# Optimization experiments

Hardware: AMD Instinct MI355X
Metric: run time of the kernel (lower is better)

## Reference

```python
import jax, jax.numpy as jnp
import numpy as np

GAMMA = 0.99  # init kwarg


def _discounted_returns(ep_rs):
    # reversed running_add = running_add*gamma + r, emitted per step
    def step(carry, r):
        carry = carry * GAMMA + r
        return carry, carry
    _, out = jax.lax.scan(step, jnp.float32(0.0), ep_rs, reverse=True)
    return out  # [T]


def setup_inputs() -> dict:
    key = jax.random.key(0)
    k1, k2, k3 = jax.random.split(key, 3)
    T, A = 2097152, 18
    weight = jax.random.normal(k1, (T, A), dtype=jnp.float32)
    ep_rs = jax.random.normal(k2, (T,), dtype=jnp.float32)
    ep_as = jax.random.randint(k3, (T,), 0, A, dtype=jnp.int64)
    return {"weight": weight, "ep_rs": ep_rs, "ep_as": ep_as}


def reference(weight, ep_rs, ep_as):
    d = _discounted_returns(ep_rs)
    d = d - jnp.mean(d)
    # cross_entropy with reduction='none': -log_softmax(weight)[t, ep_as[t]]
    logp = jax.nn.log_softmax(weight, axis=-1)  # [T, A]
    neg_log_prob = -jnp.take_along_axis(logp, ep_as[:, None], axis=-1)[:, 0]  # [T]
    return jnp.mean(neg_log_prob * d)
```

## Files before the change

kernel.cpp:

```cpp
#include <hip/hip_runtime.h>
#include <math.h>

#define T_TOTAL 2097152
#define A_DIM   18
#define GAMMA_D 0.99

#define CHUNK 256
#define NC    (T_TOTAL / CHUNK)
#define KTR   14

#define NB_MAIN 2048

__global__ void k_local(const float* __restrict__ r, double* __restrict__ L) {
    const int tid  = blockIdx.x * blockDim.x + threadIdx.x;
    const int c    = tid >> 6;
    const int lane = tid & 63;
    const float4 v = ((const float4*)r)[(size_t)c * 64 + lane];
    const double g = GAMMA_D;
    double w = pow(g, (double)(4 * lane)) *
               ((double)v.x + g * ((double)v.y + g * ((double)v.z + g * (double)v.w)));
    #pragma unroll
    for (int off = 32; off > 0; off >>= 1) w += __shfl_down(w, off, 64);
    if (lane == 0) L[c] = w;
}

__global__ void k_carry(const double* __restrict__ L, double* __restrict__ carry,
                        double G) {
    const int c = blockIdx.x * blockDim.x + threadIdx.x;
    double acc = 0.0, w = 1.0;
    #pragma unroll
    for (int m = 0; m < KTR; ++m) {
        int idx = c + 1 + m;
        if (idx < NC) acc += w * L[idx];
        w *= G;
    }
    carry[c] = acc;
}

__launch_bounds__(256)
__global__ void k_main(const float* __restrict__ wgt, const int* __restrict__ act,
                       const float* __restrict__ r, const double* __restrict__ carry,
                       double* __restrict__ partials) {
    __shared__ float  lds[CHUNK * A_DIM];
    __shared__ double ldsT[4];
    __shared__ double red[12];
    const int tid  = threadIdx.x;
    const int lane = tid & 63, wv = tid >> 6;
    const double g    = GAMMA_D;
    const double p    = pow(g, (double)tid);
    const double ip   = 1.0 / p;
    const double g256 = pow(g, 256.0);
    double s_d = 0.0, s_n = 0.0, s_nd = 0.0;

    for (int c = blockIdx.x; c < NC; c += gridDim.x) {
        __syncthreads();
        const float4* src = (const float4*)(wgt + (size_t)c * CHUNK * A_DIM);
        float4* dst = (float4*)lds;
        #pragma unroll
        for (int i = 0; i < 5; ++i) {
            int idx = tid + 256 * i;
            if (idx < CHUNK * A_DIM / 4) dst[idx] = src[idx];
        }
        const int row = c * CHUNK + tid;
        double ss = p * (double)r[row];
        #pragma unroll
        for (int off = 1; off < 64; off <<= 1) {
            double v = __shfl_down(ss, off, 64);
            ss += (lane + off < 64) ? v : 0.0;
        }
        if (lane == 0) ldsT[wv] = ss;
        __syncthreads();
        double tail = 0.0;
        #pragma unroll
        for (int m = 0; m < 4; ++m)
            if (m > wv) tail += ldsT[m];
        const double dval = ip * (ss + tail + g256 * carry[c]);
        const float* wr = lds + tid * A_DIM;
        float mx = wr[0];
        #pragma unroll
        for (int j = 1; j < A_DIM; ++j) mx = fmaxf(mx, wr[j]);
        float s = 0.0f;
        #pragma unroll
        for (int j = 0; j < A_DIM; ++j) s += expf(wr[j] - mx);
        const float nlp = mx + logf(s) - wr[act[row]];
        s_d  += dval;
        s_n  += (double)nlp;
        s_nd += (double)nlp * dval;
    }

    #pragma unroll
    for (int off = 32; off > 0; off >>= 1) {
        s_d  += __shfl_down(s_d,  off, 64);
        s_n  += __shfl_down(s_n,  off, 64);
        s_nd += __shfl_down(s_nd, off, 64);
    }
    if (lane == 0) { red[wv*3+0] = s_d; red[wv*3+1] = s_n; red[wv*3+2] = s_nd; }
    __syncthreads();
    if (tid == 0) {
        double a = 0.0, b = 0.0, cc = 0.0;
        #pragma unroll
        for (int i = 0; i < 4; ++i) { a += red[i*3]; b += red[i*3+1]; cc += red[i*3+2]; }
        partials[blockIdx.x*3+0] = a;
        partials[blockIdx.x*3+1] = b;
        partials[blockIdx.x*3+2] = cc;
    }
}

__global__ void k_final(const double* __restrict__ partials, float* __restrict__ out) {
    __shared__ double red[12];
    const int tid = threadIdx.x;
    double a = 0.0, b = 0.0, c = 0.0;
    for (int i = tid; i < NB_MAIN; i += 256) {
        a += partials[i*3+0];
        b += partials[i*3+1];
        c += partials[i*3+2];
    }
    #pragma unroll
    for (int off = 32; off > 0; off >>= 1) {
        a += __shfl_down(a, off, 64);
        b += __shfl_down(b, off, 64);
        c += __shfl_down(c, off, 64);
    }
    const int lane = tid & 63, wv = tid >> 6;
    if (lane == 0) { red[wv*3+0] = a; red[wv*3+1] = b; red[wv*3+2] = c; }
    __syncthreads();
    if (tid == 0) {
        double A_ = 0.0, B_ = 0.0, C_ = 0.0;
        #pragma unroll
        for (int i = 0; i < 4; ++i) { A_ += red[i*3]; B_ += red[i*3+1]; C_ += red[i*3+2]; }
        const double invT = 1.0 / (double)T_TOTAL;
        out[0] = (float)((C_ - (A_ * invT) * B_) * invT);
    }
}

extern "C" void kernel_launch(void* const* d_in, const int* in_sizes, int n_in,
                              void* d_out, int out_size, void* d_ws, size_t ws_size,
                              hipStream_t stream) {
    const float* weight = (const float*)d_in[0];
    const float* ep_rs  = (const float*)d_in[1];
    const int*   ep_as  = (const int*)  d_in[2];
    float* out = (float*)d_out;

    char* ws = (char*)d_ws;
    double* L        = (double*)(ws);
    double* carry    = (double*)(ws + (1 << 16));
    double* partials = (double*)(ws + (2 << 16));

    const double G = pow(GAMMA_D, (double)CHUNK);

    k_local <<<T_TOTAL / 4 / 256, 256, 0, stream>>>(ep_rs, L);
    k_carry <<<NC / 256,          256, 0, stream>>>(L, carry, G);
    k_main  <<<NB_MAIN,           256, 0, stream>>>(weight, ep_as, ep_rs, carry, partials);
    k_final <<<1,                 256, 0, stream>>>(partials, out);
}
```

Before: 234.2 us.

## Fold carry computation into main kernel and fuse final reduction via last-block atomic

Removes the separate carry kernel: each thread in the main kernel recomputes the chunk carry from the per-chunk local sums L, using a 14-term truncated sum. It also removes the final reduction kernel by having the last block to finish, detected through an atomic counter reset in k_local, reduce the partials. The launch count drops from four to two, at the cost of redundant per-thread loads of L in every chunk iteration plus a threadfence and atomic per block.

```diff
diff --git a/kernel.cpp b/kernel.cpp
--- a/kernel.cpp
+++ b/kernel.cpp
@@ -11,8 +11,10 @@
 
 #define NB_MAIN 2048
 
-__global__ void k_local(const float* __restrict__ r, double* __restrict__ L) {
+__global__ void k_local(const float* __restrict__ r, double* __restrict__ L,
+                        unsigned int* __restrict__ done) {
     const int tid  = blockIdx.x * blockDim.x + threadIdx.x;
+    if (tid == 0) *done = 0u;
     const int c    = tid >> 6;
     const int lane = tid & 63;
     const float4 v = ((const float4*)r)[(size_t)c * 64 + lane];
@@ -24,26 +26,16 @@
     if (lane == 0) L[c] = w;
 }
 
-__global__ void k_carry(const double* __restrict__ L, double* __restrict__ carry,
-                        double G) {
-    const int c = blockIdx.x * blockDim.x + threadIdx.x;
-    double acc = 0.0, w = 1.0;
-    #pragma unroll
-    for (int m = 0; m < KTR; ++m) {
-        int idx = c + 1 + m;
-        if (idx < NC) acc += w * L[idx];
-        w *= G;
-    }
-    carry[c] = acc;
-}
-
 __launch_bounds__(256)
 __global__ void k_main(const float* __restrict__ wgt, const int* __restrict__ act,
-                       const float* __restrict__ r, const double* __restrict__ carry,
-                       double* __restrict__ partials) {
+                       const float* __restrict__ r, const double* __restrict__ L,
+                       double* __restrict__ partials,
+                       unsigned int* __restrict__ done,
+                       float* __restrict__ out) {
     __shared__ float  lds[CHUNK * A_DIM];
     __shared__ double ldsT[4];
     __shared__ double red[12];
+    __shared__ unsigned int isLast;
     const int tid  = threadIdx.x;
     const int lane = tid & 63, wv = tid >> 6;
     const double g    = GAMMA_D;
@@ -61,6 +53,13 @@
             int idx = tid + 256 * i;
             if (idx < CHUNK * A_DIM / 4) dst[idx] = src[idx];
         }
+        double cy = 0.0, gw = 1.0;
+        #pragma unroll
+        for (int m = 0; m < KTR; ++m) {
+            int idx = c + 1 + m;
+            if (idx < NC) cy += gw * L[idx];
+            gw *= g256;
+        }
         const int row = c * CHUNK + tid;
         double ss = p * (double)r[row];
         #pragma unroll
@@ -74,7 +73,7 @@
         #pragma unroll
         for (int m = 0; m < 4; ++m)
             if (m > wv) tail += ldsT[m];
-        const double dval = ip * (ss + tail + g256 * carry[c]);
+        const double dval = ip * (ss + tail + g256 * cy);
         const float* wr = lds + tid * A_DIM;
         float mx = wr[0];
         #pragma unroll
@@ -103,33 +102,36 @@
         partials[blockIdx.x*3+0] = a;
         partials[blockIdx.x*3+1] = b;
         partials[blockIdx.x*3+2] = cc;
+        __threadfence();
+        unsigned int prev = atomicAdd(done, 1u);
+        isLast = (prev == (unsigned int)(gridDim.x - 1)) ? 1u : 0u;
     }
-}
+    __syncthreads();
 
-__global__ void k_final(const double* __restrict__ partials, float* __restrict__ out) {
-    __shared__ double red[12];
-    const int tid = threadIdx.x;
-    double a = 0.0, b = 0.0, c = 0.0;
-    for (int i = tid; i < NB_MAIN; i += 256) {
-        a += partials[i*3+0];
-        b += partials[i*3+1];
-        c += partials[i*3+2];
-    }
-    #pragma unroll
-    for (int off = 32; off > 0; off >>= 1) {
-        a += __shfl_down(a, off, 64);
-        b += __shfl_down(b, off, 64);
-        c += __shfl_down(c, off, 64);
-    }
-    const int lane = tid & 63, wv = tid >> 6;
-    if (lane == 0) { red[wv*3+0] = a; red[wv*3+1] = b; red[wv*3+2] = c; }
-    __syncthreads();
-    if (tid == 0) {
-        double A_ = 0.0, B_ = 0.0, C_ = 0.0;
+    if (isLast) {
+        __threadfence();
+        double a = 0.0, b = 0.0, c = 0.0;
+        for (int i = tid; i < NB_MAIN; i += 256) {
+            a += partials[i*3+0];
+            b += partials[i*3+1];
+            c += partials[i*3+2];
+        }
         #pragma unroll
-        for (int i = 0; i < 4; ++i) { A_ += red[i*3]; B_ += red[i*3+1]; C_ += red[i*3+2]; }
-        const double invT = 1.0 / (double)T_TOTAL;
-        out[0] = (float)((C_ - (A_ * invT) * B_) * invT);
+        for (int off = 32; off > 0; off >>= 1) {
+            a += __shfl_down(a, off, 64);
+            b += __shfl_down(b, off, 64);
+            c += __shfl_down(c, off, 64);
+        }
+        __syncthreads();
+        if (lane == 0) { red[wv*3+0] = a; red[wv*3+1] = b; red[wv*3+2] = c; }
+        __syncthreads();
+        if (tid == 0) {
+            double A_ = 0.0, B_ = 0.0, C_ = 0.0;
+            #pragma unroll
+            for (int i = 0; i < 4; ++i) { A_ += red[i*3]; B_ += red[i*3+1]; C_ += red[i*3+2]; }
+            const double invT = 1.0 / (double)T_TOTAL;
+            out[0] = (float)((C_ - (A_ * invT) * B_) * invT);
+        }
     }
 }
 
@@ -142,14 +144,11 @@
     float* out = (float*)d_out;
 
     char* ws = (char*)d_ws;
-    double* L        = (double*)(ws);
-    double* carry    = (double*)(ws + (1 << 16));
-    double* partials = (double*)(ws + (2 << 16));
+    double*       L        = (double*)(ws);
+    double*       partials = (double*)(ws + (1 << 16));
+    unsigned int* done     = (unsigned int*)(ws + (2 << 16));
 
-    const double G = pow(GAMMA_D, (double)CHUNK);
-
-    k_local <<<T_TOTAL / 4 / 256, 256, 0, stream>>>(ep_rs, L);
-    k_carry <<<NC / 256,          256, 0, stream>>>(L, carry, G);
-    k_main  <<<NB_MAIN,           256, 0, stream>>>(weight, ep_as, ep_rs, carry, partials);
-    k_final <<<1,                 256, 0, stream>>>(partials, out);
+    k_local <<<T_TOTAL / 4 / 256, 256, 0, stream>>>(ep_rs, L, done);
+    k_main  <<<NB_MAIN,           256, 0, stream>>>(weight, ep_as, ep_rs, L,
+                                                    partials, done, out);
 }
```

After: 307.9 us. 31.5% more time.

## Launch one block per chunk and replace pow with binary exponentiation

Applied to the files above, without the earlier changes.

The main kernel drops its grid-stride loop and launches one 256-thread block per 256-row chunk, so each block processes exactly one chunk and writes its own partial. The final reduction now sums one partial per chunk. Library pow calls are replaced with an 8-bit square-and-multiply helper and a hard-coded gamma^256 constant, which cuts per-thread setup cost. The change trades the old loop reuse for more blocks in flight, at the cost of a larger partials array and more launch and tail work in the final single-block reduction.

```diff
diff --git a/kernel.cpp b/kernel.cpp
--- a/kernel.cpp
+++ b/kernel.cpp
@@ -9,7 +9,15 @@
 #define NC    (T_TOTAL / CHUNK)
 #define KTR   14
 
-#define NB_MAIN 2048
+__device__ inline void pow_tid(double base, int e, double& out) {
+    double p = 1.0, b = base;
+    #pragma unroll
+    for (int bit = 0; bit < 8; ++bit) {
+        if (e & (1 << bit)) p *= b;
+        b *= b;
+    }
+    out = p;
+}
 
 __global__ void k_local(const float* __restrict__ r, double* __restrict__ L) {
     const int tid  = blockIdx.x * blockDim.x + threadIdx.x;
@@ -17,8 +25,9 @@
     const int lane = tid & 63;
     const float4 v = ((const float4*)r)[(size_t)c * 64 + lane];
     const double g = GAMMA_D;
-    double w = pow(g, (double)(4 * lane)) *
-               ((double)v.x + g * ((double)v.y + g * ((double)v.z + g * (double)v.w)));
+    double p;
+    pow_tid(g, 4 * lane, p);
+    double w = p * ((double)v.x + g * ((double)v.y + g * ((double)v.z + g * (double)v.w)));
     #pragma unroll
     for (int off = 32; off > 0; off >>= 1) w += __shfl_down(w, off, 64);
     if (lane == 0) L[c] = w;
@@ -46,47 +55,47 @@
     __shared__ double red[12];
     const int tid  = threadIdx.x;
     const int lane = tid & 63, wv = tid >> 6;
-    const double g    = GAMMA_D;
-    const double p    = pow(g, (double)tid);
-    const double ip   = 1.0 / p;
-    const double g256 = pow(g, 256.0);
-    double s_d = 0.0, s_n = 0.0, s_nd = 0.0;
+    const int c    = blockIdx.x;
+    const double g = GAMMA_D;
+    double p, ip;
+    pow_tid(g, tid, p);
+    pow_tid(1.0 / g, tid, ip);
+    const double g256 = 0.076314983205510425;
 
-    for (int c = blockIdx.x; c < NC; c += gridDim.x) {
-        __syncthreads();
-        const float4* src = (const float4*)(wgt + (size_t)c * CHUNK * A_DIM);
-        float4* dst = (float4*)lds;
-        #pragma unroll
-        for (int i = 0; i < 5; ++i) {
-            int idx = tid + 256 * i;
-            if (idx < CHUNK * A_DIM / 4) dst[idx] = src[idx];
-        }
-        const int row = c * CHUNK + tid;
-        double ss = p * (double)r[row];
-        #pragma unroll
-        for (int off = 1; off < 64; off <<= 1) {
-            double v = __shfl_down(ss, off, 64);
-            ss += (lane + off < 64) ? v : 0.0;
-        }
-        if (lane == 0) ldsT[wv] = ss;
-        __syncthreads();
-        double tail = 0.0;
-        #pragma unroll
-        for (int m = 0; m < 4; ++m)
-            if (m > wv) tail += ldsT[m];
-        const double dval = ip * (ss + tail + g256 * carry[c]);
-        const float* wr = lds + tid * A_DIM;
-        float mx = wr[0];
-        #pragma unroll
-        for (int j = 1; j < A_DIM; ++j) mx = fmaxf(mx, wr[j]);
-        float s = 0.0f;
-        #pragma unroll
-        for (int j = 0; j < A_DIM; ++j) s += expf(wr[j] - mx);
-        const float nlp = mx + logf(s) - wr[act[row]];
-        s_d  += dval;
-        s_n  += (double)nlp;
-        s_nd += (double)nlp * dval;
+    const float4* src = (const float4*)(wgt + (size_t)c * CHUNK * A_DIM);
+    float4* dst = (float4*)lds;
+    #pragma unroll
+    for (int i = 0; i < 5; ++i) {
+        int idx = tid + 256 * i;
+        if (idx < CHUNK * A_DIM / 4) dst[idx] = src[idx];
     }
+    const int row = c * CHUNK + tid;
+    double ss = p * (double)r[row];
+    #pragma unroll
+    for (int off = 1; off < 64; off <<= 1) {
+        double v = __shfl_down(ss, off, 64);
+        ss += (lane + off < 64) ? v : 0.0;
+    }
+    if (lane == 0) ldsT[wv] = ss;
+    __syncthreads();
+    double tail = 0.0;
+    #pragma unroll
+    for (int m = 0; m < 4; ++m)
+        if (m > wv) tail += ldsT[m];
+    const double dval = ip * (ss + tail + g256 * carry[c]);
+
+    const float* wr = lds + tid * A_DIM;
+    float mx = wr[0];
+    #pragma unroll
+    for (int j = 1; j < A_DIM; ++j) mx = fmaxf(mx, wr[j]);
+    float s = 0.0f;
+    #pragma unroll
+    for (int j = 0; j < A_DIM; ++j) s += expf(wr[j] - mx);
+    const float nlp = mx + logf(s) - wr[act[row]];
+
+    double s_d  = dval;
+    double s_n  = (double)nlp;
+    double s_nd = (double)nlp * dval;
 
     #pragma unroll
     for (int off = 32; off > 0; off >>= 1) {
@@ -100,9 +109,9 @@
         double a = 0.0, b = 0.0, cc = 0.0;
         #pragma unroll
         for (int i = 0; i < 4; ++i) { a += red[i*3]; b += red[i*3+1]; cc += red[i*3+2]; }
-        partials[blockIdx.x*3+0] = a;
-        partials[blockIdx.x*3+1] = b;
-        partials[blockIdx.x*3+2] = cc;
+        partials[c*3+0] = a;
+        partials[c*3+1] = b;
+        partials[c*3+2] = cc;
     }
 }
 
@@ -110,7 +119,7 @@
     __shared__ double red[12];
     const int tid = threadIdx.x;
     double a = 0.0, b = 0.0, c = 0.0;
-    for (int i = tid; i < NB_MAIN; i += 256) {
+    for (int i = tid; i < NC; i += 256) {
         a += partials[i*3+0];
         b += partials[i*3+1];
         c += partials[i*3+2];
@@ -150,6 +159,6 @@
 
     k_local <<<T_TOTAL / 4 / 256, 256, 0, stream>>>(ep_rs, L);
     k_carry <<<NC / 256,          256, 0, stream>>>(L, carry, G);
-    k_main  <<<NB_MAIN,           256, 0, stream>>>(weight, ep_as, ep_rs, carry, partials);
+    k_main  <<<NC,                256, 0, stream>>>(weight, ep_as, ep_rs, carry, partials);
     k_final <<<1,                 256, 0, stream>>>(partials, out);
 }
```

Measured after the change: 241.5 us. +3.1%, slower.
